# Kernel optimization log

Hardware: AMD Instinct MI355X
Metric: run time of the kernel (lower is better)

The kernel has to match this reference:

```python
import jax, jax.numpy as jnp
import numpy as np

EPS = 1e-5
G = 8    # groups
K = 3    # kernel_size


def bn(x, gamma, beta, mean, var):
    # inference-mode BatchNorm2d; x: (b,C,H,W), params: (C,)
    inv = gamma / jnp.sqrt(var + EPS)
    return x * inv[None, :, None, None] + (beta - mean * inv)[None, :, None, None]


def gconv1x1(x, w):
    # grouped 1x1 conv; x: (b, g*ci, H, W), w: (g, co, ci) -> (b, g*co, H, W)
    b, C, H, W = x.shape
    g, co, ci = w.shape
    xg = x.reshape(b, g, ci, H, W)
    y = jnp.einsum('bgihw,goi->bgohw', xg, w)
    return y.reshape(b, g * co, H, W)


def unfold3(x):
    # torch.nn.Unfold(k=3, stride=1, dilation=1, padding=1), reshaped to (b, C, 9, H, W)
    b, C, H, W = x.shape
    xp = jnp.pad(x, ((0, 0), (0, 0), (1, 1), (1, 1)))
    patches = [xp[:, :, i:i + H, j:j + W] for i in range(K) for j in range(K)]
    return jnp.stack(patches, axis=2)


def setup_inputs() -> dict:
    key = jax.random.key(0)
    ks = jax.random.split(key, 16)
    f = jax.random.normal
    u = jax.random.uniform
    return {
        'x':  f(ks[0], (2, 256, 128, 128), jnp.float32),
        'w1': f(ks[1], (8, 8, 32), jnp.float32) * 0.1,
        'b1': f(ks[2], (64,), jnp.float32) * 0.1,
        'g1': u(ks[3], (64,), jnp.float32, 0.5, 1.5),
        'be1': f(ks[4], (64,), jnp.float32) * 0.1,
        'm1': f(ks[5], (64,), jnp.float32) * 0.1,
        'v1': u(ks[6], (64,), jnp.float32, 0.5, 1.5),
        'w2': f(ks[7], (8, 10, 8), jnp.float32) * 0.1,
        'b2': f(ks[8], (80,), jnp.float32) * 0.1,
        'g2': u(ks[9], (80,), jnp.float32, 0.5, 1.5),
        'be2': f(ks[10], (80,), jnp.float32) * 0.1,
        'm2': f(ks[11], (80,), jnp.float32) * 0.1,
        'v2': u(ks[12], (80,), jnp.float32, 0.5, 1.5),
        'wv': f(ks[13], (8, 32, 32), jnp.float32) * 0.1,
    }


def reference(x, w1, b1, g1, be1, m1, v1, w2, b2, g2, be2, m2, v2, wv):
    b, C, H, W = x.shape
    # mask_conv: grouped 1x1 conv -> BN -> tanh -> grouped 1x1 conv -> BN
    t = jnp.tanh(bn(gconv1x1(x, w1) + b1[None, :, None, None], g1, be1, m1, v1))
    mn = bn(gconv1x1(t, w2) + b2[None, :, None, None], g2, be2, m2, v2)  # (b, G*(1+K*K), H, W)
    neighbor = mn[:, :G]          # (b, G, H, W)
    mask = mn[:, G:]              # (b, G*K*K, H, W)
    nb = unfold3(neighbor)        # (b, G, 9, H, W)
    logits = mask.reshape(b, G, K * K, H, W) + nb
    attn = jax.nn.softmax(logits, axis=2)               # (b, G, 9, H, W)
    # value path: grouped 1x1 conv (no bias) then unfold
    v = gconv1x1(x, wv)                                  # (b, C, H, W)
    vu = unfold3(v).reshape(b, G, C // G, K * K, H, W)   # (b, G, C/G, 9, H, W)
    out = jnp.einsum('bgkhw,bgckhw->bgchw', attn, vu)    # weighted sum over window
    return out.reshape(b, C, H, W)
```

## Files before the change

### kernel.cpp

```cpp
#include <hip/hip_runtime.h>

#define HW  16384
#define WD  128

#define TS   16
#define HS   18
#define HP   (HS * HS)
#define PRS  20
#define PLS  360

__device__ __forceinline__ unsigned short f2bf(float f) {
    unsigned int u = __builtin_bit_cast(unsigned int, f);
    u += 0x7FFFu + ((u >> 16) & 1u);
    return (unsigned short)(u >> 16);
}
__device__ __forceinline__ float bf2f(unsigned int s) {
    return __builtin_bit_cast(float, (s & 0xFFFFu) << 16);
}
__device__ __forceinline__ float ftanh(float v) {
    const float e = __expf(2.0f * v);
    return 1.0f - __fdividef(2.0f, e + 1.0f);
}

__global__ __launch_bounds__(256) void la_pre(
    const float* __restrict__ x,
    const float* __restrict__ w1, const float* __restrict__ b1,
    const float* __restrict__ g1, const float* __restrict__ be1,
    const float* __restrict__ m1, const float* __restrict__ v1,
    const float* __restrict__ w2, const float* __restrict__ b2,
    const float* __restrict__ g2, const float* __restrict__ be2,
    const float* __restrict__ m2, const float* __restrict__ v2,
    const float* __restrict__ wv,
    uint4* __restrict__ v4, float* __restrict__ nb, float* __restrict__ mask)
{
    const int pix = blockIdx.x * blockDim.x + threadIdx.x;
    const int b   = blockIdx.y;
    const int p   = blockIdx.z;

    const float* xp = x + (size_t)(b * 256 + p * 32) * HW + pix;
    float xv[32];
#pragma unroll
    for (int c = 0; c < 32; ++c) xv[c] = xp[(size_t)c * HW];

    const float* w1g = w1 + p * 256;
    float tv[8];
#pragma unroll
    for (int o = 0; o < 8; ++o) {
        float a = 0.f;
#pragma unroll
        for (int ci = 0; ci < 32; ++ci) a = fmaf(xv[ci], w1g[o * 32 + ci], a);
        const int ch = p * 8 + o;
        const float inv = g1[ch] * rsqrtf(v1[ch] + 1e-5f);
        const float add = be1[ch] + (b1[ch] - m1[ch]) * inv;
        tv[o] = ftanh(fmaf(a, inv, add));
    }

#pragma unroll
    for (int o = 0; o < 10; ++o) {
        const int c = p * 10 + o;
        float a = 0.f;
#pragma unroll
        for (int i = 0; i < 8; ++i) a = fmaf(tv[i], w2[p * 80 + o * 8 + i], a);
        const float inv = g2[c] * rsqrtf(v2[c] + 1e-5f);
        const float add = be2[c] + (b2[c] - m2[c]) * inv;
        const float val = fmaf(a, inv, add);
        if (c < 8) {
            nb[(size_t)(b * 8 + c) * HW + pix] = val;
        } else {
            const int gk = c - 8, g = gk / 9, k = gk - 9 * g;
            mask[((size_t)(b * 8 + g) * 9 + k) * HW + pix] = val;
        }
    }

    const float* wvp = wv + p * 1024;
#pragma unroll
    for (int c8 = 0; c8 < 4; ++c8) {
        float ov[8];
#pragma unroll
        for (int j = 0; j < 8; ++j) {
            float a = 0.f;
#pragma unroll
            for (int ci = 0; ci < 32; ++ci)
                a = fmaf(xv[ci], wvp[(c8 * 8 + j) * 32 + ci], a);
            ov[j] = a;
        }
        uint4 u;
        u.x = (unsigned)f2bf(ov[0]) | ((unsigned)f2bf(ov[1]) << 16);
        u.y = (unsigned)f2bf(ov[2]) | ((unsigned)f2bf(ov[3]) << 16);
        u.z = (unsigned)f2bf(ov[4]) | ((unsigned)f2bf(ov[5]) << 16);
        u.w = (unsigned)f2bf(ov[6]) | ((unsigned)f2bf(ov[7]) << 16);
        v4[((size_t)((b * 8 + p) * 4) + c8) * HW + pix] = u;
    }
}

__global__ __launch_bounds__(256, 4) void la_attn(
    const uint4* __restrict__ v4, const float* __restrict__ nb,
    const float* __restrict__ mask, float* __restrict__ out)
{
    __shared__ ushort4 vt[8 * PLS];
    __shared__ float   nbs[PLS];

    const int tid  = threadIdx.x;
    const int bg   = blockIdx.x;
    const int tile = blockIdx.y;
    const int b    = bg >> 3, g = bg & 7;
    const int ty0  = (tile >> 3) * TS;
    const int tx0  = (tile & 7) * TS;

    const int cy  = tid >> 4, cx = tid & 15;
    const int iy  = ty0 + cy, ix = tx0 + cx;
    const int pix = iy * WD + ix;
    const float* mp = mask + (size_t)(b * 8 + g) * 9 * HW + pix;
    float mk[9];
#pragma unroll
    for (int k = 0; k < 9; ++k) mk[k] = mp[(size_t)k * HW];

    const uint4* vg  = v4 + (size_t)((b * 8 + g) * 4) * HW;
    const float* nbp = nb + (size_t)(b * 8 + g) * HW;
    for (int hp = tid; hp < HP; hp += 256) {
        const int hy = hp / HS, hx = hp - hy * HS;
        const int hiy = ty0 + hy - 1, hix = tx0 + hx - 1;
        const int slot = hy * PRS + hx;
        if (((unsigned)hiy < 128u) && ((unsigned)hix < 128u)) {
            const int po = hiy * WD + hix;
            nbs[slot] = nbp[po];
#pragma unroll
            for (int c8 = 0; c8 < 4; ++c8) {
                const uint4 u = vg[(size_t)c8 * HW + po];
                vt[(2 * c8 + 0) * PLS + slot] = make_ushort4(
                    (unsigned short)u.x, (unsigned short)(u.x >> 16),
                    (unsigned short)u.y, (unsigned short)(u.y >> 16));
                vt[(2 * c8 + 1) * PLS + slot] = make_ushort4(
                    (unsigned short)u.z, (unsigned short)(u.z >> 16),
                    (unsigned short)u.w, (unsigned short)(u.w >> 16));
            }
        } else {
            const ushort4 z = make_ushort4(0, 0, 0, 0);
#pragma unroll
            for (int c4 = 0; c4 < 8; ++c4) vt[c4 * PLS + slot] = z;
            nbs[slot] = 0.f;
        }
    }
    __syncthreads();

    float lg[9];
    float mx = -1e30f;
#pragma unroll
    for (int k = 0; k < 9; ++k) {
        lg[k] = mk[k] + nbs[(cy + k / 3) * PRS + (cx + k % 3)];
        mx = fmaxf(mx, lg[k]);
    }
    float ssum = 0.f;
#pragma unroll
    for (int k = 0; k < 9; ++k) { lg[k] = __expf(lg[k] - mx); ssum += lg[k]; }
    const float rs = 1.f / ssum;

    float s[32];
#pragma unroll
    for (int c = 0; c < 32; ++c) s[c] = 0.f;
#pragma unroll
    for (int k = 0; k < 9; ++k) {
        const int slot = (cy + k / 3) * PRS + (cx + k % 3);
        const float e = lg[k];
#pragma unroll
        for (int c4 = 0; c4 < 8; ++c4) {
            const ushort4 vv = vt[c4 * PLS + slot];
            s[c4 * 4 + 0] = fmaf(e, bf2f(vv.x), s[c4 * 4 + 0]);
            s[c4 * 4 + 1] = fmaf(e, bf2f(vv.y), s[c4 * 4 + 1]);
            s[c4 * 4 + 2] = fmaf(e, bf2f(vv.z), s[c4 * 4 + 2]);
            s[c4 * 4 + 3] = fmaf(e, bf2f(vv.w), s[c4 * 4 + 3]);
        }
    }

    float* og = out + (size_t)(b * 256 + g * 32) * HW + pix;
#pragma unroll 8
    for (int o = 0; o < 32; ++o)
        __builtin_nontemporal_store(s[o] * rs, og + (size_t)o * HW);
}

extern "C" void kernel_launch(void* const* d_in, const int* in_sizes, int n_in,
                              void* d_out, int out_size, void* d_ws, size_t ws_size,
                              hipStream_t stream)
{
    const float* x   = (const float*)d_in[0];
    const float* w1  = (const float*)d_in[1];
    const float* b1  = (const float*)d_in[2];
    const float* g1  = (const float*)d_in[3];
    const float* be1 = (const float*)d_in[4];
    const float* m1  = (const float*)d_in[5];
    const float* v1  = (const float*)d_in[6];
    const float* w2  = (const float*)d_in[7];
    const float* b2  = (const float*)d_in[8];
    const float* g2  = (const float*)d_in[9];
    const float* be2 = (const float*)d_in[10];
    const float* m2  = (const float*)d_in[11];
    const float* v2  = (const float*)d_in[12];
    const float* wv  = (const float*)d_in[13];

    float* out = (float*)d_out;

    uint4* v4  = (uint4*)d_ws;
    float* nbw = (float*)((char*)d_ws + (size_t)64 * HW * 16);
    float* msk = nbw + (size_t)16 * HW;

    dim3 blk(256);
    dim3 gpre(HW / 256, 2, 8);
    dim3 gatt(16, 64);

    hipLaunchKernelGGL(la_pre, gpre, blk, 0, stream,
                       x, w1, b1, g1, be1, m1, v1, w2, b2, g2, be2, m2, v2,
                       wv, v4, nbw, msk);
    hipLaunchKernelGGL(la_attn, gatt, blk, 0, stream,
                       v4, nbw, msk, out);
}
```

Baseline: 142.8 us.

## Replace LDS halo tiling in attention kernel with direct cached global loads

The attention kernel no longer stages a 18x18 halo tile of bf16 values and neighbor logits in shared memory with a barrier. Each thread now reads its 3x3 neighborhood directly from global memory with bounds checks, relying on L1/L2 caches for reuse, and blocks become 256-pixel row strips. This removes the LDS staging, the repacking and the sync, but it issues nine 16-byte global loads per channel chunk per pixel instead of one, and the row-strip layout makes reuse across rows depend on cache hits.

Result: no change. 140.6 us (-1.6%).

```diff
diff --git a/kernel.cpp b/kernel.cpp
--- a/kernel.cpp
+++ b/kernel.cpp
@@ -2,12 +2,6 @@
 
 #define HW  16384
 #define WD  128
-
-#define TS   16
-#define HS   18
-#define HP   (HS * HS)
-#define PRS  20
-#define PLS  360
 
 __device__ __forceinline__ unsigned short f2bf(float f) {
     unsigned int u = __builtin_bit_cast(unsigned int, f);
@@ -93,61 +87,27 @@
     }
 }
 
-__global__ __launch_bounds__(256, 4) void la_attn(
+__global__ __launch_bounds__(256) void la_attn(
     const uint4* __restrict__ v4, const float* __restrict__ nb,
     const float* __restrict__ mask, float* __restrict__ out)
 {
-    __shared__ ushort4 vt[8 * PLS];
-    __shared__ float   nbs[PLS];
+    const int pix = blockIdx.x * blockDim.x + threadIdx.x;
+    const int bg  = blockIdx.y;
+    const int b   = bg >> 3, g = bg & 7;
+    const int iy  = pix >> 7, ix = pix & 127;
 
-    const int tid  = threadIdx.x;
-    const int bg   = blockIdx.x;
-    const int tile = blockIdx.y;
-    const int b    = bg >> 3, g = bg & 7;
-    const int ty0  = (tile >> 3) * TS;
-    const int tx0  = (tile & 7) * TS;
-
-    const int cy  = tid >> 4, cx = tid & 15;
-    const int iy  = ty0 + cy, ix = tx0 + cx;
-    const int pix = iy * WD + ix;
-    const float* mp = mask + (size_t)(b * 8 + g) * 9 * HW + pix;
-    float mk[9];
-#pragma unroll
-    for (int k = 0; k < 9; ++k) mk[k] = mp[(size_t)k * HW];
-
-    const uint4* vg  = v4 + (size_t)((b * 8 + g) * 4) * HW;
-    const float* nbp = nb + (size_t)(b * 8 + g) * HW;
-    for (int hp = tid; hp < HP; hp += 256) {
-        const int hy = hp / HS, hx = hp - hy * HS;
-        const int hiy = ty0 + hy - 1, hix = tx0 + hx - 1;
-        const int slot = hy * PRS + hx;
-        if (((unsigned)hiy < 128u) && ((unsigned)hix < 128u)) {
-            const int po = hiy * WD + hix;
-            nbs[slot] = nbp[po];
-#pragma unroll
-            for (int c8 = 0; c8 < 4; ++c8) {
-                const uint4 u = vg[(size_t)c8 * HW + po];
-                vt[(2 * c8 + 0) * PLS + slot] = make_ushort4(
-                    (unsigned short)u.x, (unsigned short)(u.x >> 16),
-                    (unsigned short)u.y, (unsigned short)(u.y >> 16));
-                vt[(2 * c8 + 1) * PLS + slot] = make_ushort4(
-                    (unsigned short)u.z, (unsigned short)(u.z >> 16),
-                    (unsigned short)u.w, (unsigned short)(u.w >> 16));
-            }
-        } else {
-            const ushort4 z = make_ushort4(0, 0, 0, 0);
-#pragma unroll
-            for (int c4 = 0; c4 < 8; ++c4) vt[c4 * PLS + slot] = z;
-            nbs[slot] = 0.f;
-        }
-    }
-    __syncthreads();
+    const float* mp  = mask + ((size_t)(b * 8 + g) * 9) * HW + pix;
+    const float* nbp = nb   + (size_t)(b * 8 + g) * HW + pix;
+    const uint4* vg  = v4   + ((size_t)(b * 8 + g) * 4) * HW + pix;
 
     float lg[9];
     float mx = -1e30f;
 #pragma unroll
     for (int k = 0; k < 9; ++k) {
-        lg[k] = mk[k] + nbs[(cy + k / 3) * PRS + (cx + k % 3)];
+        const int dy = k / 3 - 1, dx = k % 3 - 1;
+        const bool ok = ((unsigned)(iy + dy) < 128u) && ((unsigned)(ix + dx) < 128u);
+        const float nv = ok ? nbp[dy * WD + dx] : 0.f;
+        lg[k] = mp[(size_t)k * HW] + nv;
         mx = fmaxf(mx, lg[k]);
     }
     float ssum = 0.f;
@@ -160,15 +120,23 @@
     for (int c = 0; c < 32; ++c) s[c] = 0.f;
 #pragma unroll
     for (int k = 0; k < 9; ++k) {
-        const int slot = (cy + k / 3) * PRS + (cx + k % 3);
-        const float e = lg[k];
+        const int dy = k / 3 - 1, dx = k % 3 - 1;
+        const bool ok = ((unsigned)(iy + dy) < 128u) && ((unsigned)(ix + dx) < 128u);
+        if (ok) {
+            const int off = dy * WD + dx;
+            const float e = lg[k];
 #pragma unroll
-        for (int c4 = 0; c4 < 8; ++c4) {
-            const ushort4 vv = vt[c4 * PLS + slot];
-            s[c4 * 4 + 0] = fmaf(e, bf2f(vv.x), s[c4 * 4 + 0]);
-            s[c4 * 4 + 1] = fmaf(e, bf2f(vv.y), s[c4 * 4 + 1]);
-            s[c4 * 4 + 2] = fmaf(e, bf2f(vv.z), s[c4 * 4 + 2]);
-            s[c4 * 4 + 3] = fmaf(e, bf2f(vv.w), s[c4 * 4 + 3]);
+            for (int c8 = 0; c8 < 4; ++c8) {
+                const uint4 u = vg[(size_t)c8 * HW + off];
+                s[c8 * 8 + 0] = fmaf(e, bf2f(u.x),       s[c8 * 8 + 0]);
+                s[c8 * 8 + 1] = fmaf(e, bf2f(u.x >> 16), s[c8 * 8 + 1]);
+                s[c8 * 8 + 2] = fmaf(e, bf2f(u.y),       s[c8 * 8 + 2]);
+                s[c8 * 8 + 3] = fmaf(e, bf2f(u.y >> 16), s[c8 * 8 + 3]);
+                s[c8 * 8 + 4] = fmaf(e, bf2f(u.z),       s[c8 * 8 + 4]);
+                s[c8 * 8 + 5] = fmaf(e, bf2f(u.z >> 16), s[c8 * 8 + 5]);
+                s[c8 * 8 + 6] = fmaf(e, bf2f(u.w),       s[c8 * 8 + 6]);
+                s[c8 * 8 + 7] = fmaf(e, bf2f(u.w >> 16), s[c8 * 8 + 7]);
+            }
         }
     }
 
@@ -205,7 +173,7 @@
 
     dim3 blk(256);
     dim3 gpre(HW / 256, 2, 8);
-    dim3 gatt(16, 64);
+    dim3 gatt(HW / 256, 16);
 
     hipLaunchKernelGGL(la_pre, gpre, blk, 0, stream,
                        x, w1, b1, g1, be1, m1, v1, w2, b2, g2, be2, m2, v2,
```
